# Performance work log

Hardware: AMD Instinct MI355X
Metric: run time of the kernel (lower is better)

Reference implementation:

```python
import jax, jax.numpy as jnp
import numpy as np

MUL = 8                       # multiplicity of 0e and 1o in node irreps
INV_SQRT3 = float(1.0 / np.sqrt(3.0))   # wigner 3j (1,1,0) / (0,1,1) / (1,0,1) coefficient
# e3nn path normalization ('component' irrep norm, 'element' path norm):
# alpha(out) = sqrt((2*l_out+1) / sum_paths(mul1*mul2)); two 64-element paths per output irrep -> 128
A_SCALAR = float(np.sqrt(1.0 / 128.0))  # l_out = 0
A_VECTOR = float(np.sqrt(3.0 / 128.0))  # l_out = 1
SQRT2 = float(np.sqrt(2.0))             # e3nn normalize2mom factor for relu

N_NODES, N_EDGES, NUM_BASIS, HIDDEN = 50000, 800000, 8, 256
WEIGHT_NUMEL = 4 * MUL * MUL  # 4 CG paths, uvw weights each (MUL,1,MUL)


def setup_inputs() -> dict:
    k = jax.random.split(jax.random.key(0), 7)
    node_features = jax.random.normal(k[0], (N_NODES, 4 * MUL), jnp.float32)  # [8x0e | 8x1o]
    edge_src = jax.random.randint(k[1], (N_EDGES,), 0, N_NODES)
    edge_dst = jax.random.randint(k[2], (N_EDGES,), 0, N_NODES)
    edge_sh = jax.random.normal(k[3], (N_EDGES, 4), jnp.float32)             # [1x0e | 1x1o]
    edge_scalars = jax.random.uniform(k[4], (N_EDGES, NUM_BASIS), jnp.float32)
    fc_w1 = jax.random.normal(k[5], (NUM_BASIS, HIDDEN), jnp.float32)
    fc_w2 = jax.random.normal(k[6], (HIDDEN, WEIGHT_NUMEL), jnp.float32)
    return dict(node_features=node_features, edge_src=edge_src, edge_dst=edge_dst,
                edge_sh=edge_sh, edge_scalars=edge_scalars, fc_w1=fc_w1, fc_w2=fc_w2)


def reference(node_features, edge_src, edge_dst, edge_sh, edge_scalars, fc_w1, fc_w2):
    N = node_features.shape[0]
    E = edge_src.shape[0]

    # --- radial MLP -> per-edge TP weights (e3nn FullyConnectedNet, weights / sqrt(fan_in), relu*sqrt(2))
    h = jax.nn.relu(edge_scalars @ (fc_w1 * (1.0 / np.sqrt(NUM_BASIS)))) * SQRT2   # (E, 256)
    w = (h @ (fc_w2 * (1.0 / np.sqrt(HIDDEN)))).reshape(E, 4, MUL, MUL)            # (E, 4, u, w)

    # --- gather source node features and split irreps
    x = node_features[edge_src]                 # (E, 32)
    s1 = x[:, :MUL]                             # (E, 8)    8x0e
    v1 = x[:, MUL:].reshape(E, MUL, 3)          # (E, 8, 3) 8x1o
    s2 = edge_sh[:, 0]                          # (E,)      1x0e
    v2 = edge_sh[:, 1:4]                        # (E, 3)    1x1o

    # --- fully connected CG tensor product (4 paths)
    # path0: 0e x 0e -> 0e ; path1: 1o x 1o -> 0e (dot / sqrt(3))
    out_s = A_SCALAR * (jnp.einsum('eu,euw->ew', s1 * s2[:, None], w[:, 0])
                        + INV_SQRT3 * jnp.einsum('eui,ei,euw->ew', v1, v2, w[:, 1]))
    # path2: 0e x 1o -> 1o ; path3: 1o x 0e -> 1o (both coeff 1/sqrt(3))
    out_v = (A_VECTOR * INV_SQRT3) * (jnp.einsum('eu,euw,ei->ewi', s1, w[:, 2], v2)
                                      + jnp.einsum('eui,euw->ewi', v1 * s2[:, None, None], w[:, 3]))

    edge_features = jnp.concatenate([out_s, out_v.reshape(E, 3 * MUL)], axis=1)    # (E, 32)

    # --- scatter-sum to destination nodes, divide by sqrt(avg_degree)
    node_out = jax.ops.segment_sum(edge_features, edge_dst, num_segments=N)
    return node_out * (1.0 / np.sqrt(E / N))
```

## Files before the change

### kernel.cpp

```cpp
#include <hip/hip_runtime.h>
#include <hip/hip_bf16.h>

#define E_TOTAL 800000
#define BM 128
#define NKC 16
#define WT 34

static constexpr float INV_SQRT3_C = 0.57735026918962576f;
static constexpr float CS = 0.0013810679320049758f;

typedef __attribute__((ext_vector_type(8)))  __bf16 bf16x8;
typedef __attribute__((ext_vector_type(8)))  short  s16x8;
typedef __attribute__((ext_vector_type(16))) float  f32x16;

union frag_u { s16x8 s; bf16x8 b; };

typedef __attribute__((address_space(3))) unsigned int lds_u32;
typedef const __attribute__((address_space(1))) unsigned int glb_u32;

__device__ __forceinline__ void split_bf16(float v, short& hi, short& lo) {
    unsigned u  = __float_as_uint(v);
    unsigned hb = (u + 0x7fffu + ((u >> 16) & 1u)) & 0xffff0000u;
    hi = (short)(hb >> 16);
    float r = v - __uint_as_float(hb);
    unsigned u2 = __float_as_uint(r);
    lo = (short)((u2 + 0x7fffu + ((u2 >> 16) & 1u)) >> 16);
}

__global__ void split_w2_kernel(const float* __restrict__ w2, short* __restrict__ w2f) {
    const int idx  = blockIdx.x * 256 + threadIdx.x;
    const int i    = idx & 7;
    const int nloc = (idx >> 3) & 127;
    const int g    = (idx >> 10) & 1;
    const int hl   = (idx >> 11) & 1;
    const int kc   = (idx >> 12) & 15;
    const int pass = idx >> 16;
    const int k = kc * 16 + g * 8 + i;
    const int n = pass * 128 + nloc;
    short hi, lo;
    split_bf16(w2[k * 256 + n], hi, lo);
    w2f[idx] = hl ? lo : hi;
}

__global__ __launch_bounds__(256, 3)
void conv_mfma_kernel(const float* __restrict__ nf,
                      const int*   __restrict__ esrc,
                      const int*   __restrict__ edst,
                      const float* __restrict__ esh,
                      const float* __restrict__ escal,
                      const float* __restrict__ w1,
                      const short* __restrict__ w2f,
                      float* __restrict__ out)
{
    __shared__ __align__(16) char smem[45056];
    short* Bbuf  = (short*)smem;
    float* wtile = (float*)smem;
    float* xtile = (float*)(smem + 17408);
    float* shtl  = (float*)(smem + 34816);
    float* w1l   = (float*)(smem + 36864);

    const int t  = threadIdx.x;
    const int l  = t & 63;
    const int wv = t >> 6;
    const int e0 = blockIdx.x * BM;

    {
        const int e = t >> 1, h2 = t & 1;
        const int src = esrc[e0 + e];
        const float* xp = nf + (size_t)src * 32 + h2 * 16;
        float* dp = xtile + e * WT + h2 * 16;
        #pragma unroll
        for (int q = 0; q < 4; ++q) {
            const float4 v4 = *reinterpret_cast<const float4*>(xp + q * 4);
            *reinterpret_cast<float2*>(dp + q * 4)     = make_float2(v4.x, v4.y);
            *reinterpret_cast<float2*>(dp + q * 4 + 2) = make_float2(v4.z, v4.w);
        }
        if (t < BM) {
            const float4 s4 = *reinterpret_cast<const float4*>(esh + (size_t)(e0 + t) * 4);
            *reinterpret_cast<float4*>(shtl + t * 4) = s4;
        }
        *reinterpret_cast<float4*>(w1l + t * 8)     = *reinterpret_cast<const float4*>(w1 + t * 8);
        *reinterpret_cast<float4*>(w1l + t * 8 + 4) = *reinterpret_cast<const float4*>(w1 + t * 8 + 4);
    }

    const int erow = e0 + wv * 32 + (l & 31);
    float es[8];
    {
        const float4 a = *reinterpret_cast<const float4*>(escal + (size_t)erow * 8);
        const float4 b = *reinterpret_cast<const float4*>(escal + (size_t)erow * 8 + 4);
        es[0]=a.x; es[1]=a.y; es[2]=a.z; es[3]=a.w;
        es[4]=b.x; es[5]=b.y; es[6]=b.z; es[7]=b.w;
    }
    __syncthreads();

    auto compute_A = [&](int kc, frag_u& fh, frag_u& fl) {
        const int hb = kc * 16 + (l >> 5) * 8;
        float hv[8];
        #pragma unroll
        for (int i2 = 0; i2 < 8; ++i2) hv[i2] = 0.f;
        #pragma unroll
        for (int b = 0; b < 8; ++b) {
            const float4 wa  = *reinterpret_cast<const float4*>(w1l + b * 256 + hb);
            const float4 wb4 = *reinterpret_cast<const float4*>(w1l + b * 256 + hb + 4);
            hv[0] = fmaf(es[b], wa.x,  hv[0]);
            hv[1] = fmaf(es[b], wa.y,  hv[1]);
            hv[2] = fmaf(es[b], wa.z,  hv[2]);
            hv[3] = fmaf(es[b], wa.w,  hv[3]);
            hv[4] = fmaf(es[b], wb4.x, hv[4]);
            hv[5] = fmaf(es[b], wb4.y, hv[5]);
            hv[6] = fmaf(es[b], wb4.z, hv[6]);
            hv[7] = fmaf(es[b], wb4.w, hv[7]);
        }
        #pragma unroll
        for (int i2 = 0; i2 < 8; ++i2) {
            const float v = fmaxf(hv[i2], 0.f) * 0.5f;
            short hi, lo;
            split_bf16(v, hi, lo);
            fh.s[i2] = hi;
            fl.s[i2] = lo;
        }
    };

    const int el = t >> 3;
    const int j  = t & 7;

    for (int pass = 0; pass < 2; ++pass) {
        const short* wp = w2f + pass * 65536;

        auto stage = [&](int kc, int buf) {
            const short* src = wp + kc * 4096;
            short* dst = Bbuf + buf * 4096;
            #pragma unroll
            for (int r = 0; r < 2; ++r) {
                __builtin_amdgcn_global_load_lds((glb_u32*)(src + r * 2048 + t * 8),
                                                 (lds_u32*)(dst + r * 2048 + t * 8),
                                                 16, 0, 0);
            }
        };

        f32x16 acc[4];
        #pragma unroll
        for (int nt = 0; nt < 4; ++nt)
            #pragma unroll
            for (int q = 0; q < 16; ++q) acc[nt][q] = 0.f;

        stage(0, 0);
        frag_u Ahi, Alo;
        compute_A(0, Ahi, Alo);
        __syncthreads();

        const int bbase = (l >> 5) * 1024 + (l & 31) * 8;

        for (int kc = 0; kc < NKC; ++kc) {
            const int cur = kc & 1;
            if (kc + 1 < NKC) stage(kc + 1, cur ^ 1);

            frag_u Anh, Anl;
            if (kc + 1 < NKC) compute_A(kc + 1, Anh, Anl);

            const short* Bb = Bbuf + cur * 4096;
            #pragma unroll
            for (int nt = 0; nt < 4; ++nt) {
                frag_u Bhi, Blo;
                Bhi.s = *reinterpret_cast<const s16x8*>(Bb + bbase + nt * 256);
                Blo.s = *reinterpret_cast<const s16x8*>(Bb + 2048 + bbase + nt * 256);
                acc[nt] = __builtin_amdgcn_mfma_f32_32x32x16_bf16(Ahi.b, Bhi.b, acc[nt], 0, 0, 0);
                acc[nt] = __builtin_amdgcn_mfma_f32_32x32x16_bf16(Alo.b, Bhi.b, acc[nt], 0, 0, 0);
                acc[nt] = __builtin_amdgcn_mfma_f32_32x32x16_bf16(Ahi.b, Blo.b, acc[nt], 0, 0, 0);
            }

            if (kc + 1 < NKC) { Ahi = Anh; Alo = Anl; }
            __syncthreads();
        }

        for (int round = 0; round < 4; ++round) {
            if (wv == round) {
                #pragma unroll
                for (int nt = 0; nt < 4; ++nt) {
                    float* bp = wtile + (nt * 32 + (l & 31)) * WT + (l >> 5) * 4;
                    #pragma unroll
                    for (int q = 0; q < 4; ++q) {
                        *reinterpret_cast<float2*>(bp + q * 8)     = make_float2(acc[nt][q*4+0], acc[nt][q*4+1]);
                        *reinterpret_cast<float2*>(bp + q * 8 + 2) = make_float2(acc[nt][q*4+2], acc[nt][q*4+3]);
                    }
                }
            }
            __syncthreads();

            const int eg = round * 32 + el;
            const float* xr = xtile + eg * WT;
            const float s2  = shtl[eg * 4 + 0];
            const float v20 = shtl[eg * 4 + 1];
            const float v21 = shtl[eg * 4 + 2];
            const float v22 = shtl[eg * 4 + 3];
            const int dst = edst[e0 + eg];
            float* op = out + (size_t)dst * 32;

            if (pass == 0) {
                float P0 = 0.f, P1 = 0.f;
                #pragma unroll
                for (int u = 0; u < 8; ++u) {
                    const float s1 = xr[u];
                    const float a0 = xr[8 + u * 3 + 0];
                    const float a1 = xr[8 + u * 3 + 1];
                    const float a2 = xr[8 + u * 3 + 2];
                    const float dv = a0 * v20 + a1 * v21 + a2 * v22;
                    P0 = fmaf(s1, wtile[(     u * 8 + j) * WT + el], P0);
                    P1 = fmaf(dv, wtile[(64 + u * 8 + j) * WT + el], P1);
                }
                atomicAdd(op + j, CS * (s2 * P0 + INV_SQRT3_C * P1));
            } else {
                float Q = 0.f, R0 = 0.f, R1 = 0.f, R2 = 0.f;
                #pragma unroll
                for (int u = 0; u < 8; ++u) {
                    const float s1 = xr[u];
                    const float a0 = xr[8 + u * 3 + 0];
                    const float a1 = xr[8 + u * 3 + 1];
                    const float a2 = xr[8 + u * 3 + 2];
                    const float w2v = wtile[(     u * 8 + j) * WT + el];
                    const float w3v = wtile[(64 + u * 8 + j) * WT + el];
                    Q  = fmaf(s1, w2v, Q);
                    R0 = fmaf(a0, w3v, R0);
                    R1 = fmaf(a1, w3v, R1);
                    R2 = fmaf(a2, w3v, R2);
                }
                atomicAdd(op + 8 + j * 3 + 0, CS * (Q * v20 + s2 * R0));
                atomicAdd(op + 8 + j * 3 + 1, CS * (Q * v21 + s2 * R1));
                atomicAdd(op + 8 + j * 3 + 2, CS * (Q * v22 + s2 * R2));
            }
            __syncthreads();
        }
    }
}

extern "C" void kernel_launch(void* const* d_in, const int* in_sizes, int n_in,
                              void* d_out, int out_size, void* d_ws, size_t ws_size,
                              hipStream_t stream) {
    const float* nf    = (const float*)d_in[0];
    const int*   esrc  = (const int*)d_in[1];
    const int*   edst  = (const int*)d_in[2];
    const float* esh   = (const float*)d_in[3];
    const float* escal = (const float*)d_in[4];
    const float* w1    = (const float*)d_in[5];
    const float* w2    = (const float*)d_in[6];
    float* out  = (float*)d_out;
    short* w2f  = (short*)d_ws;

    hipMemsetAsync(d_out, 0, (size_t)out_size * sizeof(float), stream);
    split_w2_kernel<<<512, 256, 0, stream>>>(w2, w2f);
    conv_mfma_kernel<<<E_TOTAL / BM, 256, 0, stream>>>(
        nf, esrc, edst, esh, escal, w1, w2f, out);
}
```

Measured before the change: 550.2 us.

## Swap MFMA operand order so the TP epilogue reads weights straight from accumulators

The MFMA operands are swapped (weights as A, hidden activations as B) so each lane's accumulator holds the per-edge TP weights for its own edge. The epilogue then contracts directly from registers instead of spilling the accumulator tile to LDS in four serialized rounds with barriers. The two passes become one continuous staged pipeline, prefetching the first pass-2 tile during the pass-1 epilogue, and the ReLU's 0.5 scale is folded into the edge scalars. Each thread now issues its atomics for 4 output channels per edge instead of 1 channel across 8 threads. This changes the atomic access pattern and adds register pressure.

```diff
diff --git a/kernel.cpp b/kernel.cpp
--- a/kernel.cpp
+++ b/kernel.cpp
@@ -3,8 +3,7 @@
 
 #define E_TOTAL 800000
 #define BM 128
-#define NKC 16
-#define WT 34
+#define WT 36
 
 static constexpr float INV_SQRT3_C = 0.57735026918962576f;
 static constexpr float CS = 0.0013810679320049758f;
@@ -54,8 +53,7 @@
 {
     __shared__ __align__(16) char smem[45056];
     short* Bbuf  = (short*)smem;
-    float* wtile = (float*)smem;
-    float* xtile = (float*)(smem + 17408);
+    float* xtile = (float*)(smem + 16384);
     float* shtl  = (float*)(smem + 34816);
     float* w1l   = (float*)(smem + 36864);
 
@@ -64,21 +62,30 @@
     const int wv = t >> 6;
     const int e0 = blockIdx.x * BM;
 
+    auto stage = [&](int s, int buf) {
+        const short* src = w2f + (size_t)s * 4096;
+        short* dst = Bbuf + buf * 4096;
+        #pragma unroll
+        for (int r = 0; r < 2; ++r)
+            __builtin_amdgcn_global_load_lds((glb_u32*)(src + r * 2048 + t * 8),
+                                             (lds_u32*)(dst + r * 2048 + t * 8),
+                                             16, 0, 0);
+    };
+
+    stage(0, 0);
+
     {
         const int e = t >> 1, h2 = t & 1;
         const int src = esrc[e0 + e];
         const float* xp = nf + (size_t)src * 32 + h2 * 16;
         float* dp = xtile + e * WT + h2 * 16;
         #pragma unroll
-        for (int q = 0; q < 4; ++q) {
-            const float4 v4 = *reinterpret_cast<const float4*>(xp + q * 4);
-            *reinterpret_cast<float2*>(dp + q * 4)     = make_float2(v4.x, v4.y);
-            *reinterpret_cast<float2*>(dp + q * 4 + 2) = make_float2(v4.z, v4.w);
-        }
-        if (t < BM) {
-            const float4 s4 = *reinterpret_cast<const float4*>(esh + (size_t)(e0 + t) * 4);
-            *reinterpret_cast<float4*>(shtl + t * 4) = s4;
-        }
+        for (int q = 0; q < 4; ++q)
+            *reinterpret_cast<float4*>(dp + q * 4) =
+                *reinterpret_cast<const float4*>(xp + q * 4);
+        if (t < BM)
+            *reinterpret_cast<float4*>(shtl + t * 4) =
+                *reinterpret_cast<const float4*>(esh + (size_t)(e0 + t) * 4);
         *reinterpret_cast<float4*>(w1l + t * 8)     = *reinterpret_cast<const float4*>(w1 + t * 8);
         *reinterpret_cast<float4*>(w1l + t * 8 + 4) = *reinterpret_cast<const float4*>(w1 + t * 8 + 4);
     }
@@ -88,9 +95,10 @@
     {
         const float4 a = *reinterpret_cast<const float4*>(escal + (size_t)erow * 8);
         const float4 b = *reinterpret_cast<const float4*>(escal + (size_t)erow * 8 + 4);
-        es[0]=a.x; es[1]=a.y; es[2]=a.z; es[3]=a.w;
-        es[4]=b.x; es[5]=b.y; es[6]=b.z; es[7]=b.w;
-    }
+        es[0]=a.x*0.5f; es[1]=a.y*0.5f; es[2]=a.z*0.5f; es[3]=a.w*0.5f;
+        es[4]=b.x*0.5f; es[5]=b.y*0.5f; es[6]=b.z*0.5f; es[7]=b.w*0.5f;
+    }
+
     __syncthreads();
 
     auto compute_A = [&](int kc, frag_u& fh, frag_u& fl) {
@@ -113,7 +121,7 @@
         }
         #pragma unroll
         for (int i2 = 0; i2 < 8; ++i2) {
-            const float v = fmaxf(hv[i2], 0.f) * 0.5f;
+            const float v = fmaxf(hv[i2], 0.f);
             short hi, lo;
             split_bf16(v, hi, lo);
             fh.s[i2] = hi;
@@ -121,114 +129,122 @@
         }
     };
 
-    const int el = t >> 3;
-    const int j  = t & 7;
-
-    for (int pass = 0; pass < 2; ++pass) {
-        const short* wp = w2f + pass * 65536;
-
-        auto stage = [&](int kc, int buf) {
-            const short* src = wp + kc * 4096;
-            short* dst = Bbuf + buf * 4096;
-            #pragma unroll
-            for (int r = 0; r < 2; ++r) {
-                __builtin_amdgcn_global_load_lds((glb_u32*)(src + r * 2048 + t * 8),
-                                                 (lds_u32*)(dst + r * 2048 + t * 8),
-                                                 16, 0, 0);
-            }
-        };
-
-        f32x16 acc[4];
+    frag_u Ahi, Alo;
+    compute_A(0, Ahi, Alo);
+
+    f32x16 acc[4];
+    #pragma unroll
+    for (int nt = 0; nt < 4; ++nt)
+        #pragma unroll
+        for (int q = 0; q < 16; ++q) acc[nt][q] = 0.f;
+
+    const int bbase = (l >> 5) * 1024 + (l & 31) * 8;
+
+    for (int s = 0; s < 16; ++s) {
+        const int cur = s & 1;
+        stage(s + 1, cur ^ 1);
+        frag_u Anh, Anl;
+        compute_A((s + 1) & 15, Anh, Anl);
+        const short* Bb = Bbuf + cur * 4096;
+        #pragma unroll
+        for (int nt = 0; nt < 4; ++nt) {
+            frag_u Wh, Wl;
+            Wh.s = *reinterpret_cast<const s16x8*>(Bb + bbase + nt * 256);
+            Wl.s = *reinterpret_cast<const s16x8*>(Bb + 2048 + bbase + nt * 256);
+            acc[nt] = __builtin_amdgcn_mfma_f32_32x32x16_bf16(Wh.b, Ahi.b, acc[nt], 0, 0, 0);
+            acc[nt] = __builtin_amdgcn_mfma_f32_32x32x16_bf16(Wh.b, Alo.b, acc[nt], 0, 0, 0);
+            acc[nt] = __builtin_amdgcn_mfma_f32_32x32x16_bf16(Wl.b, Ahi.b, acc[nt], 0, 0, 0);
+        }
+        Ahi = Anh; Alo = Anl;
+        if (s < 15) __syncthreads();
+    }
+
+    const int eg  = wv * 32 + (l & 31);
+    const int hi_ = l >> 5;
+    const float* xr = xtile + eg * WT;
+    const int dst = edst[e0 + eg];
+    float* op = out + (size_t)dst * 32;
+    const float s2  = shtl[eg * 4 + 0];
+    const float v20 = shtl[eg * 4 + 1];
+    const float v21 = shtl[eg * 4 + 2];
+    const float v22 = shtl[eg * 4 + 3];
+
+    {
+        float dv[8];
+        #pragma unroll
+        for (int u = 0; u < 8; ++u)
+            dv[u] = xr[8 + u*3] * v20 + xr[8 + u*3 + 1] * v21 + xr[8 + u*3 + 2] * v22;
+        float P0[4] = {0.f,0.f,0.f,0.f}, P1[4] = {0.f,0.f,0.f,0.f};
         #pragma unroll
         for (int nt = 0; nt < 4; ++nt)
             #pragma unroll
-            for (int q = 0; q < 16; ++q) acc[nt][q] = 0.f;
-
-        stage(0, 0);
-        frag_u Ahi, Alo;
-        compute_A(0, Ahi, Alo);
-        __syncthreads();
-
-        const int bbase = (l >> 5) * 1024 + (l & 31) * 8;
-
-        for (int kc = 0; kc < NKC; ++kc) {
-            const int cur = kc & 1;
-            if (kc + 1 < NKC) stage(kc + 1, cur ^ 1);
-
-            frag_u Anh, Anl;
-            if (kc + 1 < NKC) compute_A(kc + 1, Anh, Anl);
-
-            const short* Bb = Bbuf + cur * 4096;
+            for (int uu = 0; uu < 4; ++uu) {
+                const int q = nt * 4 + uu, u = q & 7;
+                const float s1u = xr[u];
+                #pragma unroll
+                for (int jj = 0; jj < 4; ++jj) {
+                    const float w = acc[nt][uu * 4 + jj];
+                    if (q < 8) P0[jj] = fmaf(s1u,   w, P0[jj]);
+                    else       P1[jj] = fmaf(dv[u], w, P1[jj]);
+                }
+            }
+        #pragma unroll
+        for (int jj = 0; jj < 4; ++jj)
+            atomicAdd(op + jj + 4 * hi_, CS * (s2 * P0[jj] + INV_SQRT3_C * P1[jj]));
+    }
+
+    #pragma unroll
+    for (int nt = 0; nt < 4; ++nt)
+        #pragma unroll
+        for (int q = 0; q < 16; ++q) acc[nt][q] = 0.f;
+
+    __syncthreads();
+
+    for (int s = 16; s < 32; ++s) {
+        const int cur = s & 1;
+        if (s < 31) stage(s + 1, cur ^ 1);
+        frag_u Anh, Anl;
+        if (s < 31) compute_A((s + 1) & 15, Anh, Anl);
+        const short* Bb = Bbuf + cur * 4096;
+        #pragma unroll
+        for (int nt = 0; nt < 4; ++nt) {
+            frag_u Wh, Wl;
+            Wh.s = *reinterpret_cast<const s16x8*>(Bb + bbase + nt * 256);
+            Wl.s = *reinterpret_cast<const s16x8*>(Bb + 2048 + bbase + nt * 256);
+            acc[nt] = __builtin_amdgcn_mfma_f32_32x32x16_bf16(Wh.b, Ahi.b, acc[nt], 0, 0, 0);
+            acc[nt] = __builtin_amdgcn_mfma_f32_32x32x16_bf16(Wh.b, Alo.b, acc[nt], 0, 0, 0);
+            acc[nt] = __builtin_amdgcn_mfma_f32_32x32x16_bf16(Wl.b, Ahi.b, acc[nt], 0, 0, 0);
+        }
+        if (s < 31) { Ahi = Anh; Alo = Anl; __syncthreads(); }
+    }
+
+    {
+        float Q[4]  = {0.f,0.f,0.f,0.f};
+        float R0[4] = {0.f,0.f,0.f,0.f}, R1[4] = {0.f,0.f,0.f,0.f}, R2[4] = {0.f,0.f,0.f,0.f};
+        #pragma unroll
+        for (int nt = 0; nt < 4; ++nt)
             #pragma unroll
-            for (int nt = 0; nt < 4; ++nt) {
-                frag_u Bhi, Blo;
-                Bhi.s = *reinterpret_cast<const s16x8*>(Bb + bbase + nt * 256);
-                Blo.s = *reinterpret_cast<const s16x8*>(Bb + 2048 + bbase + nt * 256);
-                acc[nt] = __builtin_amdgcn_mfma_f32_32x32x16_bf16(Ahi.b, Bhi.b, acc[nt], 0, 0, 0);
-                acc[nt] = __builtin_amdgcn_mfma_f32_32x32x16_bf16(Alo.b, Bhi.b, acc[nt], 0, 0, 0);
-                acc[nt] = __builtin_amdgcn_mfma_f32_32x32x16_bf16(Ahi.b, Blo.b, acc[nt], 0, 0, 0);
-            }
-
-            if (kc + 1 < NKC) { Ahi = Anh; Alo = Anl; }
-            __syncthreads();
-        }
-
-        for (int round = 0; round < 4; ++round) {
-            if (wv == round) {
+            for (int uu = 0; uu < 4; ++uu) {
+                const int q = nt * 4 + uu, u = q & 7;
+                const float s1u = xr[u];
+                const float a0 = xr[8 + u*3], a1 = xr[8 + u*3 + 1], a2 = xr[8 + u*3 + 2];
                 #pragma unroll
-                for (int nt = 0; nt < 4; ++nt) {
-                    float* bp = wtile + (nt * 32 + (l & 31)) * WT + (l >> 5) * 4;
-                    #pragma unroll
-                    for (int q = 0; q < 4; ++q) {
-                        *reinterpret_cast<float2*>(bp + q * 8)     = make_float2(acc[nt][q*4+0], acc[nt][q*4+1]);
-                        *reinterpret_cast<float2*>(bp + q * 8 + 2) = make_float2(acc[nt][q*4+2], acc[nt][q*4+3]);
+                for (int jj = 0; jj < 4; ++jj) {
+                    const float w = acc[nt][uu * 4 + jj];
+                    if (q < 8) Q[jj] = fmaf(s1u, w, Q[jj]);
+                    else {
+                        R0[jj] = fmaf(a0, w, R0[jj]);
+                        R1[jj] = fmaf(a1, w, R1[jj]);
+                        R2[jj] = fmaf(a2, w, R2[jj]);
                     }
                 }
             }
-            __syncthreads();
-
-            const int eg = round * 32 + el;
-            const float* xr = xtile + eg * WT;
-            const float s2  = shtl[eg * 4 + 0];
-            const float v20 = shtl[eg * 4 + 1];
-            const float v21 = shtl[eg * 4 + 2];
-            const float v22 = shtl[eg * 4 + 3];
-            const int dst = edst[e0 + eg];
-            float* op = out + (size_t)dst * 32;
-
-            if (pass == 0) {
-                float P0 = 0.f, P1 = 0.f;
-                #pragma unroll
-                for (int u = 0; u < 8; ++u) {
-                    const float s1 = xr[u];
-                    const float a0 = xr[8 + u * 3 + 0];
-                    const float a1 = xr[8 + u * 3 + 1];
-                    const float a2 = xr[8 + u * 3 + 2];
-                    const float dv = a0 * v20 + a1 * v21 + a2 * v22;
-                    P0 = fmaf(s1, wtile[(     u * 8 + j) * WT + el], P0);
-                    P1 = fmaf(dv, wtile[(64 + u * 8 + j) * WT + el], P1);
-                }
-                atomicAdd(op + j, CS * (s2 * P0 + INV_SQRT3_C * P1));
-            } else {
-                float Q = 0.f, R0 = 0.f, R1 = 0.f, R2 = 0.f;
-                #pragma unroll
-                for (int u = 0; u < 8; ++u) {
-                    const float s1 = xr[u];
-                    const float a0 = xr[8 + u * 3 + 0];
-                    const float a1 = xr[8 + u * 3 + 1];
-                    const float a2 = xr[8 + u * 3 + 2];
-                    const float w2v = wtile[(     u * 8 + j) * WT + el];
-                    const float w3v = wtile[(64 + u * 8 + j) * WT + el];
-                    Q  = fmaf(s1, w2v, Q);
-                    R0 = fmaf(a0, w3v, R0);
-                    R1 = fmaf(a1, w3v, R1);
-                    R2 = fmaf(a2, w3v, R2);
-                }
-                atomicAdd(op + 8 + j * 3 + 0, CS * (Q * v20 + s2 * R0));
-                atomicAdd(op + 8 + j * 3 + 1, CS * (Q * v21 + s2 * R1));
-                atomicAdd(op + 8 + j * 3 + 2, CS * (Q * v22 + s2 * R2));
-            }
-            __syncthreads();
+        #pragma unroll
+        for (int jj = 0; jj < 4; ++jj) {
+            const int j = jj + 4 * hi_;
+            atomicAdd(op + 8 + j * 3 + 0, CS * (Q[jj] * v20 + s2 * R0[jj]));
+            atomicAdd(op + 8 + j * 3 + 1, CS * (Q[jj] * v21 + s2 * R1[jj]));
+            atomicAdd(op + 8 + j * 3 + 2, CS * (Q[jj] * v22 + s2 * R2[jj]));
         }
     }
 }
```

After: 1.135 ms. 106% more time.
